# Performance work log

Hardware: AMD Instinct MI355X
Metric: run time of the kernel (lower is better)

## Reference

```python
import jax, jax.numpy as jnp
import numpy as np

EMBED_DIM = 1024
NUM_HEADS = 16
HEAD_DIM = EMBED_DIM // NUM_HEADS


def setup_inputs() -> dict:
    key = jax.random.key(0)
    k1, k2, k3, k4 = jax.random.split(key, 4)
    B, S, D = 2, 2048, EMBED_DIM
    x = jax.random.normal(k1, (B, S, D), dtype=jnp.float32)
    xpos = jax.random.randint(k2, (B, S), 0, 2048, dtype=jnp.int32)
    # torch nn.Linear weights: [out_features, in_features]; qkv_bias=False -> no qkv bias
    qkv_w = jax.random.normal(k3, (3 * D, D), dtype=jnp.float32) * (D ** -0.5)
    proj_w = jax.random.normal(k4, (D, D), dtype=jnp.float32) * (D ** -0.5)
    proj_b = jnp.zeros((D,), dtype=jnp.float32)
    return {"x": x, "xpos": xpos, "qkv_w": qkv_w, "proj_w": proj_w, "proj_b": proj_b}


def reference(x, xpos, qkv_w, proj_w, proj_b):
    # rope is None, dropout rates are 0, so xpos is unused and dropout is identity.
    B, S, D = x.shape
    H, hd = NUM_HEADS, D // NUM_HEADS
    scale = hd ** -0.5

    qkv = x @ qkv_w.T                                   # [B, S, 3D]
    qkv = qkv.reshape(B, S, 3, H, hd)
    qkv = jnp.transpose(qkv, (0, 3, 2, 1, 4))           # [B, H, 3, S, hd]
    q, k, v = qkv[:, :, 0], qkv[:, :, 1], qkv[:, :, 2]  # each [B, H, S, hd]

    scores = jnp.einsum("bhqd,bhkd->bhqk", q, k) * scale  # [B, H, S, S]
    probs = jax.nn.softmax(scores, axis=-1)
    out = jnp.einsum("bhqk,bhkd->bhqd", probs, v)         # [B, H, S, hd]

    out = jnp.transpose(out, (0, 2, 1, 3)).reshape(B, S, D)
    out = out @ proj_w.T + proj_b
    return out
```

## Files before the change

### kernel.cpp

```cpp
#include <hip/hip_runtime.h>


typedef __bf16 bf16_8 __attribute__((ext_vector_type(8)));
typedef __bf16 bf16_4 __attribute__((ext_vector_type(4)));
typedef __bf16 bf16_2 __attribute__((ext_vector_type(2)));
typedef float floatx4 __attribute__((ext_vector_type(4)));
typedef float floatx16 __attribute__((ext_vector_type(16)));
typedef unsigned uintx4 __attribute__((ext_vector_type(4)));

#define MFMA16 __builtin_amdgcn_mfma_f32_16x16x32_bf16
#define MFMA32 __builtin_amdgcn_mfma_f32_32x32x16_bf16
#define CSCALE 0.1803368801111204f
#define EXP2R  __builtin_amdgcn_exp2f

__device__ __forceinline__ void gld16(const __bf16* g, __bf16* l) {
    __builtin_amdgcn_global_load_lds(
        (const __attribute__((address_space(1))) void*)g,
        (__attribute__((address_space(3))) void*)l, 16, 0, 0);
}

__device__ __forceinline__ unsigned pk_bf16(float a, float b) {
    bf16_2 t;
    t[0] = (__bf16)a; t[1] = (__bf16)b;
    return __builtin_bit_cast(unsigned, t);
}

__device__ __forceinline__ void pl32swap(unsigned& a, unsigned& b) {
    __asm__ __volatile__("v_permlane32_swap_b32 %0, %1" : "+v"(a), "+v"(b));
}

__global__ __launch_bounds__(256) void cvt_all(
    const float* __restrict__ x, const float* __restrict__ w1,
    const float* __restrict__ w2,
    __bf16* __restrict__ xb, __bf16* __restrict__ w1b, __bf16* __restrict__ w2b)
{
    const int i = blockIdx.x * 256 + threadIdx.x;
    const float* src; __bf16* dst; int off;
    if (i < (1 << 20))                  { src = x;  dst = xb;  off = i; }
    else if (i < (1 << 20) + 786432)    { src = w1; dst = w1b; off = i - (1 << 20); }
    else                                { src = w2; dst = w2b; off = i - (1 << 20) - 786432; }
    float4 v = ((const float4*)src)[off];
    bf16_4 o;
    o[0] = (__bf16)v.x; o[1] = (__bf16)v.y; o[2] = (__bf16)v.z; o[3] = (__bf16)v.w;
    ((bf16_4*)dst)[off] = o;
}

__global__ __launch_bounds__(512) void qkv_gemm(
    const __bf16* __restrict__ X, const __bf16* __restrict__ W,
    __bf16* __restrict__ q_ws, __bf16* __restrict__ k_ws, __bf16* __restrict__ vt_ws)
{
    __shared__ __align__(16) __bf16 S[2][2][128 * 64];

    const int tid = threadIdx.x, lane = tid & 63;
    const int half = tid >> 8, htid = tid & 255;
    const int wvh = (tid >> 6) & 3;
    const int quad = lane >> 4, l15 = lane & 15;
    const int wm = (wvh >> 1) * 64, wn = (wvh & 1) * 64;
    const int m0 = blockIdx.y * 128, n0 = blockIdx.x * 128;
    const int c = n0 >> 10;

    const __bf16* Abase;
    const __bf16* Bbase;
    if (c == 2) { Abase = X + (size_t)m0 * 1024; Bbase = W + (size_t)n0 * 1024; }
    else        { Abase = W + (size_t)n0 * 1024; Bbase = X + (size_t)m0 * 1024; }
    Abase += half * 512;
    Bbase += half * 512;

    __bf16* As = S[half][0];
    __bf16* Bs = S[half][1];
    floatx4 acc[4][4] = {};

    for (int k0 = 0; k0 < 512; k0 += 64) {
        __syncthreads();
#pragma unroll
        for (int it = 0; it < 4; ++it) {
            int cc = it * 256 + htid;
            int row = cc >> 3, kc = cc & 7;
            gld16(Abase + row * 1024 + k0 + ((kc ^ (row & 7)) * 8), &As[cc * 8]);
        }
#pragma unroll
        for (int it = 0; it < 4; ++it) {
            int cc = it * 256 + htid;
            int row = cc >> 3, kc = cc & 7;
            gld16(Bbase + row * 1024 + k0 + ((kc ^ (row & 7)) * 8), &Bs[cc * 8]);
        }
        __syncthreads();

#pragma unroll
        for (int ks = 0; ks < 2; ++ks) {
            bf16_8 af[4], bf[4];
#pragma unroll
            for (int mt = 0; mt < 4; ++mt) {
                int r = wm + mt * 16 + l15;
                af[mt] = *(const bf16_8*)&As[r * 64 + (((ks * 4 + quad) ^ (r & 7)) * 8)];
            }
#pragma unroll
            for (int nt = 0; nt < 4; ++nt) {
                int r = wn + nt * 16 + l15;
                bf[nt] = *(const bf16_8*)&Bs[r * 64 + (((ks * 4 + quad) ^ (r & 7)) * 8)];
            }
#pragma unroll
            for (int mt = 0; mt < 4; ++mt)
#pragma unroll
                for (int nt = 0; nt < 4; ++nt)
                    acc[mt][nt] = MFMA16(af[mt], bf[nt], acc[mt][nt], 0, 0, 0);
        }
    }

    __syncthreads();
    float* comb = (float*)S;
    if (half == 1) {
#pragma unroll
        for (int mt = 0; mt < 4; ++mt)
#pragma unroll
            for (int nt = 0; nt < 4; ++nt)
                *(floatx4*)&comb[((mt * 4 + nt) * 256 + htid) * 4] = acc[mt][nt];
    }
    __syncthreads();
    if (half != 0) return;

#pragma unroll
    for (int mt = 0; mt < 4; ++mt)
#pragma unroll
        for (int nt = 0; nt < 4; ++nt)
            acc[mt][nt] += *(const floatx4*)&comb[((mt * 4 + nt) * 256 + htid) * 4];

    if (c == 2) {
#pragma unroll
        for (int mt = 0; mt < 4; ++mt) {
            const int mbase = m0 + wm + mt * 16 + quad * 4;
            const int b = mbase >> 11, s = mbase & 2047;
#pragma unroll
            for (int nt = 0; nt < 4; ++nt) {
                const int n = n0 + wn + nt * 16 + l15;
                const int h = (n >> 6) & 15, d = n & 63;
                bf16_4 pk;
#pragma unroll
                for (int r = 0; r < 4; ++r) pk[r] = (__bf16)acc[mt][nt][r];
                *(bf16_4*)&vt_ws[((b * 16 + h) * 64 + d) * 2048 + s] = pk;
            }
        }
    } else {
        __bf16* dst = (c == 0) ? q_ws : k_ws;
        const float scale = (c == 1) ? CSCALE : 1.0f;
#pragma unroll
        for (int mt = 0; mt < 4; ++mt) {
            const int nn = n0 + wm + mt * 16 + quad * 4;
            const int h = (nn >> 6) & 15, d0 = nn & 63;
#pragma unroll
            for (int nt = 0; nt < 4; ++nt) {
                const int token = m0 + wn + nt * 16 + l15;
                const int b = token >> 11, s = token & 2047;
                bf16_4 pk;
#pragma unroll
                for (int r = 0; r < 4; ++r) pk[r] = (__bf16)(acc[mt][nt][r] * scale);
                *(bf16_4*)&dst[((b * 16 + h) * 2048 + s) * 64 + d0] = pk;
            }
        }
    }
}

__global__ __launch_bounds__(256) void attn_kernel(
    const __bf16* __restrict__ q_ws, const __bf16* __restrict__ k_ws,
    const __bf16* __restrict__ vt_ws, __bf16* __restrict__ attn_ws)
{
    __shared__ __align__(16) __bf16 Ks [2][64 * 64];
    __shared__ __align__(16) __bf16 Vts[2][64 * 64];

    const int tid = threadIdx.x, lane = tid & 63, w = tid >> 6;
    const int l31 = lane & 31, hi = lane >> 5;
    const int bh = blockIdx.x, qt = blockIdx.y;
    const int q0 = qt * 128;

    const __bf16* qp  = q_ws  + (size_t)bh * (2048 * 64);
    const __bf16* kp  = k_ws  + (size_t)bh * (2048 * 64);
    const __bf16* vtp = vt_ws + (size_t)bh * (64 * 2048);

    const int srow = tid >> 3, skc = tid & 7;
    const int sw   = (skc ^ (srow & 7)) * 8;
    const __bf16* kb = kp  + (size_t)srow * 64 + sw;
    const __bf16* vb = vtp + (size_t)srow * 2048 + sw;
    const int ldsoff = tid * 8;

    bf16_8 qf[4];
    {
        const int qrow = q0 + w * 32 + l31;
#pragma unroll
        for (int s = 0; s < 4; ++s)
            qf[s] = *(const bf16_8*)&qp[qrow * 64 + s * 16 + hi * 8];
    }

    floatx16 oacc[2] = {};
    float lsum = 0.f;

    gld16(kb,             &Ks [0][ldsoff]);
    gld16(kb + 32 * 64,   &Ks [0][ldsoff + 2048]);
    gld16(vb,             &Vts[0][ldsoff]);
    gld16(vb + 32 * 2048, &Vts[0][ldsoff + 2048]);
    __syncthreads();

#pragma unroll 2
    for (int kt = 0; kt < 32; ++kt) {
        const int cur = kt & 1;
        if (kt < 31) {
            const __bf16* kn = kb + (size_t)(kt + 1) * 4096;
            const __bf16* vn = vb + (size_t)(kt + 1) * 64;
            gld16(kn,             &Ks [cur ^ 1][ldsoff]);
            gld16(kn + 32 * 64,   &Ks [cur ^ 1][ldsoff + 2048]);
            gld16(vn,             &Vts[cur ^ 1][ldsoff]);
            gld16(vn + 32 * 2048, &Vts[cur ^ 1][ldsoff + 2048]);
        }
        const __bf16* Kb = Ks[cur];
        const __bf16* Vb = Vts[cur];

        floatx16 sacc[2] = {};
        __builtin_amdgcn_s_setprio(1);
#pragma unroll
        for (int s = 0; s < 4; ++s) {
            const int kc = s * 2 + hi;
#pragma unroll
            for (int t = 0; t < 2; ++t) {
                const int row = t * 32 + l31;
                bf16_8 kf = *(const bf16_8*)&Kb[row * 64 + ((kc ^ (row & 7)) * 8)];
                sacc[t] = MFMA32(kf, qf[s], sacc[t], 0, 0, 0);
            }
        }
        __builtin_amdgcn_s_setprio(0);

        unsigned D[2][4][2];
#pragma unroll
        for (int t = 0; t < 2; ++t)
#pragma unroll
            for (int j = 0; j < 4; ++j)
#pragma unroll
                for (int e = 0; e < 2; ++e) {
                    float pa = EXP2R(sacc[t][j * 4 + e * 2]);
                    float pb = EXP2R(sacc[t][j * 4 + e * 2 + 1]);
                    lsum += pa + pb;
                    D[t][j][e] = pk_bf16(pa, pb);
                }

        __builtin_amdgcn_s_setprio(1);
#pragma unroll
        for (int s = 0; s < 4; ++s) {
            const int t = s >> 1, b2 = (s & 1) * 2;
            unsigned x0 = D[t][b2][0], y0 = D[t][b2 + 1][0];
            unsigned x1 = D[t][b2][1], y1 = D[t][b2 + 1][1];
            pl32swap(x0, y0);
            pl32swap(x1, y1);
            uintx4 u; u[0] = x0; u[1] = x1; u[2] = y0; u[3] = y1;
            const bf16_8 pf = __builtin_bit_cast(bf16_8, u);
            const int kc = s * 2 + hi;
#pragma unroll
            for (int dt = 0; dt < 2; ++dt) {
                const int row = dt * 32 + l31;
                bf16_8 vf = *(const bf16_8*)&Vb[row * 64 + ((kc ^ (row & 7)) * 8)];
                oacc[dt] = MFMA32(vf, pf, oacc[dt], 0, 0, 0);
            }
        }
        __builtin_amdgcn_s_setprio(0);

        if (kt < 31) {
            __asm__ __volatile__("s_waitcnt vmcnt(0)" ::: "memory");
            __syncthreads();
        }
    }

    const int b = bh >> 4, h = bh & 15;
    const float lpart = __shfl_xor(lsum, 32, 64);
    const float inv_l = 1.0f / (lsum + lpart);
    const int token = b * 2048 + q0 + w * 32 + l31;
#pragma unroll
    for (int dt = 0; dt < 2; ++dt)
#pragma unroll
        for (int g = 0; g < 4; ++g) {
            bf16_4 ok;
#pragma unroll
            for (int r = 0; r < 4; ++r)
                ok[r] = (__bf16)(oacc[dt][g * 4 + r] * inv_l);
            *(bf16_4*)&attn_ws[(size_t)token * 1024 + h * 64 + dt * 32 + g * 8 + hi * 4] = ok;
        }
}

__device__ __forceinline__ void proj_stage(
    const __bf16* __restrict__ A, const __bf16* __restrict__ Bp,
    int k0, __bf16* As, __bf16* Bs, int tid)
{
#pragma unroll
    for (int it = 0; it < 4; ++it) {
        int cc = it * 256 + tid;
        int row = cc >> 3, kc = cc & 7;
        gld16(A + row * 1024 + k0 + ((kc ^ (row & 7)) * 8), &As[cc * 8]);
    }
#pragma unroll
    for (int it = 0; it < 2; ++it) {
        int cc = it * 256 + tid;
        int row = cc >> 3, kc = cc & 7;
        gld16(Bp + row * 1024 + k0 + ((kc ^ (row & 7)) * 8), &Bs[cc * 8]);
    }
}

__global__ __launch_bounds__(256) void proj_gemm(
    const __bf16* __restrict__ Ain, const __bf16* __restrict__ W,
    const float* __restrict__ bias, float* __restrict__ out)
{
    __shared__ __align__(16) __bf16 As[2][128 * 64];
    __shared__ __align__(16) __bf16 Bs[2][64 * 64];
    floatx4 acc[4][2] = {};
    const int m0 = blockIdx.y * 128, n0 = blockIdx.x * 64;

    const int tid = threadIdx.x, lane = tid & 63, wv = tid >> 6;
    const int quad = lane >> 4, l15 = lane & 15;
    const int wm = (wv >> 1) * 64, wn = (wv & 1) * 32;

    const __bf16* A  = Ain + (size_t)m0 * 1024;
    const __bf16* Bp = W   + (size_t)n0 * 1024;

    proj_stage(A, Bp, 0, As[0], Bs[0], tid);
    __syncthreads();

#pragma unroll 2
    for (int kk = 0; kk < 16; ++kk) {
        const int cur = kk & 1;
        if (kk < 15)
            proj_stage(A, Bp, (kk + 1) * 64, As[cur ^ 1], Bs[cur ^ 1], tid);

        const __bf16* Ab = As[cur];
        const __bf16* Bb = Bs[cur];
#pragma unroll
        for (int ks = 0; ks < 2; ++ks) {
            bf16_8 af[4], bf[2];
#pragma unroll
            for (int mt = 0; mt < 4; ++mt) {
                int r = wm + mt * 16 + l15;
                af[mt] = *(const bf16_8*)&Ab[r * 64 + (((ks * 4 + quad) ^ (r & 7)) * 8)];
            }
#pragma unroll
            for (int nt = 0; nt < 2; ++nt) {
                int r = wn + nt * 16 + l15;
                bf[nt] = *(const bf16_8*)&Bb[r * 64 + (((ks * 4 + quad) ^ (r & 7)) * 8)];
            }
#pragma unroll
            for (int mt = 0; mt < 4; ++mt)
#pragma unroll
                for (int nt = 0; nt < 2; ++nt)
                    acc[mt][nt] = MFMA16(af[mt], bf[nt], acc[mt][nt], 0, 0, 0);
        }

        if (kk < 15) {
            __asm__ __volatile__("s_waitcnt vmcnt(0)" ::: "memory");
            __syncthreads();
        }
    }

    float bv[2];
#pragma unroll
    for (int nt = 0; nt < 2; ++nt) bv[nt] = bias[n0 + wn + nt * 16 + l15];

#pragma unroll
    for (int mt = 0; mt < 4; ++mt) {
        const int m = m0 + wm + mt * 16 + quad * 4;
#pragma unroll
        for (int nt = 0; nt < 2; ++nt) {
            const int n = n0 + wn + nt * 16 + l15;
#pragma unroll
            for (int r = 0; r < 4; ++r)
                out[(size_t)(m + r) * 1024 + n] = acc[mt][nt][r] + bv[nt];
        }
    }
}

extern "C" void kernel_launch(void* const* d_in, const int* in_sizes, int n_in,
                              void* d_out, int out_size, void* d_ws, size_t ws_size,
                              hipStream_t stream)
{
    const float* x      = (const float*)d_in[0];
    const float* qkv_w  = (const float*)d_in[2];
    const float* proj_w = (const float*)d_in[3];
    const float* proj_b = (const float*)d_in[4];
    float* out = (float*)d_out;

    const size_t SZ   = 4096 * 1024;
    const size_t WQKV = 3072 * 1024;
    const size_t WPRJ = 1024 * 1024;

    __bf16* xb      = (__bf16*)d_ws;
    __bf16* qkvwb   = xb + SZ;
    __bf16* projwb  = qkvwb + WQKV;
    __bf16* q_ws    = projwb + WPRJ;
    __bf16* k_ws    = q_ws + SZ;
    __bf16* vt_ws   = k_ws + SZ;
    __bf16* attn_ws = vt_ws + SZ;

    cvt_all<<<dim3(8192), 256, 0, stream>>>(x, qkv_w, proj_w, xb, qkvwb, projwb);
    qkv_gemm  <<<dim3(24, 32), 512, 0, stream>>>(xb, qkvwb, q_ws, k_ws, vt_ws);
    attn_kernel<<<dim3(32, 16), 256, 0, stream>>>(q_ws, k_ws, vt_ws, attn_ws);
    proj_gemm <<<dim3(16, 32), 256, 0, stream>>>(attn_ws, projwb, proj_b, out);
}
```

Baseline: 188.6 us.

## Pre-swizzle K/V into MFMA fragment layout and load directly to registers

The QKV GEMM now writes K and V^T in a layout that matches the per-lane MFMA operand fragments. The attention kernel can then read K and V straight from global memory into registers, with K software-pipelined one tile ahead, instead of staging them through LDS behind barriers. The QKV GEMM also drops its two-half split-K design with an LDS reduction in favour of a 256-thread double-buffered K loop. The attention grid is reordered so consecutive blocks share the same head. In exchange, every wave loads its own copy of K and V from global/L2 with no LDS sharing, and register pressure rises.

New measurement: 182.3 us. 3.4% less time.

```diff
diff --git a/kernel.cpp b/kernel.cpp
--- a/kernel.cpp
+++ b/kernel.cpp
@@ -45,17 +45,15 @@
     ((bf16_4*)dst)[off] = o;
 }
 
-__global__ __launch_bounds__(512) void qkv_gemm(
+__global__ __launch_bounds__(256) void qkv_gemm(
     const __bf16* __restrict__ X, const __bf16* __restrict__ W,
     __bf16* __restrict__ q_ws, __bf16* __restrict__ k_ws, __bf16* __restrict__ vt_ws)
 {
     __shared__ __align__(16) __bf16 S[2][2][128 * 64];
 
-    const int tid = threadIdx.x, lane = tid & 63;
-    const int half = tid >> 8, htid = tid & 255;
-    const int wvh = (tid >> 6) & 3;
+    const int tid = threadIdx.x, lane = tid & 63, wv = tid >> 6;
     const int quad = lane >> 4, l15 = lane & 15;
-    const int wm = (wvh >> 1) * 64, wn = (wvh & 1) * 64;
+    const int wm = (wv >> 1) * 64, wn = (wv & 1) * 64;
     const int m0 = blockIdx.y * 128, n0 = blockIdx.x * 128;
     const int c = n0 >> 10;
 
@@ -63,29 +61,32 @@
     const __bf16* Bbase;
     if (c == 2) { Abase = X + (size_t)m0 * 1024; Bbase = W + (size_t)n0 * 1024; }
     else        { Abase = W + (size_t)n0 * 1024; Bbase = X + (size_t)m0 * 1024; }
-    Abase += half * 512;
-    Bbase += half * 512;
-
-    __bf16* As = S[half][0];
-    __bf16* Bs = S[half][1];
+
+    const int srow = tid >> 3, skc = tid & 7;
+    const int ssw  = (skc ^ (srow & 7)) * 8;
+
+#define QKV_STAGE(buf, k0)                                                     \
+    {                                                                          \
+        _Pragma("unroll")                                                      \
+        for (int itg = 0; itg < 4; ++itg) {                                    \
+            const int cc = itg * 256 + tid;                                    \
+            const int row = srow + itg * 32;                                   \
+            gld16(Abase + row * 1024 + (k0) + ssw, &S[buf][0][cc * 8]);        \
+            gld16(Bbase + row * 1024 + (k0) + ssw, &S[buf][1][cc * 8]);        \
+        }                                                                      \
+    }
+
     floatx4 acc[4][4] = {};
-
-    for (int k0 = 0; k0 < 512; k0 += 64) {
-        __syncthreads();
-#pragma unroll
-        for (int it = 0; it < 4; ++it) {
-            int cc = it * 256 + htid;
-            int row = cc >> 3, kc = cc & 7;
-            gld16(Abase + row * 1024 + k0 + ((kc ^ (row & 7)) * 8), &As[cc * 8]);
-        }
-#pragma unroll
-        for (int it = 0; it < 4; ++it) {
-            int cc = it * 256 + htid;
-            int row = cc >> 3, kc = cc & 7;
-            gld16(Bbase + row * 1024 + k0 + ((kc ^ (row & 7)) * 8), &Bs[cc * 8]);
-        }
-        __syncthreads();
-
+    QKV_STAGE(0, 0)
+    __syncthreads();
+
+#pragma unroll 1
+    for (int kk = 0; kk < 16; ++kk) {
+        const int cur = kk & 1;
+        if (kk < 15) QKV_STAGE(cur ^ 1, (kk + 1) * 64)
+
+        const __bf16* As = S[cur][0];
+        const __bf16* Bs = S[cur][1];
 #pragma unroll
         for (int ks = 0; ks < 2; ++ks) {
             bf16_8 af[4], bf[4];
@@ -105,43 +106,34 @@
                 for (int nt = 0; nt < 4; ++nt)
                     acc[mt][nt] = MFMA16(af[mt], bf[nt], acc[mt][nt], 0, 0, 0);
         }
-    }
-
-    __syncthreads();
-    float* comb = (float*)S;
-    if (half == 1) {
-#pragma unroll
-        for (int mt = 0; mt < 4; ++mt)
-#pragma unroll
-            for (int nt = 0; nt < 4; ++nt)
-                *(floatx4*)&comb[((mt * 4 + nt) * 256 + htid) * 4] = acc[mt][nt];
-    }
-    __syncthreads();
-    if (half != 0) return;
-
-#pragma unroll
-    for (int mt = 0; mt < 4; ++mt)
-#pragma unroll
-        for (int nt = 0; nt < 4; ++nt)
-            acc[mt][nt] += *(const floatx4*)&comb[((mt * 4 + nt) * 256 + htid) * 4];
+
+        if (kk < 15) {
+            __asm__ __volatile__("s_waitcnt vmcnt(0)" ::: "memory");
+            __syncthreads();
+        }
+    }
 
     if (c == 2) {
 #pragma unroll
         for (int mt = 0; mt < 4; ++mt) {
             const int mbase = m0 + wm + mt * 16 + quad * 4;
-            const int b = mbase >> 11, s = mbase & 2047;
+            const int b = mbase >> 11, key0 = mbase & 2047;
 #pragma unroll
             for (int nt = 0; nt < 4; ++nt) {
                 const int n = n0 + wn + nt * 16 + l15;
                 const int h = (n >> 6) & 15, d = n & 63;
+                const int dt = d >> 5, l31v = d & 31;
                 bf16_4 pk;
 #pragma unroll
                 for (int r = 0; r < 4; ++r) pk[r] = (__bf16)acc[mt][nt][r];
-                *(bf16_4*)&vt_ws[((b * 16 + h) * 64 + d) * 2048 + s] = pk;
+                const size_t off =
+                    (((size_t)(b * 16 + h) * 32 + (key0 >> 6)) * 2 + dt) * 2048
+                    + ((key0 >> 4) & 3) * 512
+                    + (((key0 >> 3) & 1) * 32 + l31v) * 8 + (key0 & 7);
+                *(bf16_4*)&vt_ws[off] = pk;
             }
         }
     } else {
-        __bf16* dst = (c == 0) ? q_ws : k_ws;
         const float scale = (c == 1) ? CSCALE : 1.0f;
 #pragma unroll
         for (int mt = 0; mt < 4; ++mt) {
@@ -150,37 +142,37 @@
 #pragma unroll
             for (int nt = 0; nt < 4; ++nt) {
                 const int token = m0 + wn + nt * 16 + l15;
-                const int b = token >> 11, s = token & 2047;
+                const int b = token >> 11, key = token & 2047;
                 bf16_4 pk;
 #pragma unroll
                 for (int r = 0; r < 4; ++r) pk[r] = (__bf16)(acc[mt][nt][r] * scale);
-                *(bf16_4*)&dst[((b * 16 + h) * 2048 + s) * 64 + d0] = pk;
-            }
-        }
-    }
+                if (c == 0) {
+                    *(bf16_4*)&q_ws[((size_t)(b * 16 + h) * 2048 + key) * 64 + d0] = pk;
+                } else {
+                    const size_t off =
+                        (((size_t)(b * 16 + h) * 32 + (key >> 6)) * 2 + ((key >> 5) & 1)) * 2048
+                        + (d0 >> 4) * 512
+                        + (((d0 >> 3) & 1) * 32 + (key & 31)) * 8 + (d0 & 7);
+                    *(bf16_4*)&k_ws[off] = pk;
+                }
+            }
+        }
+    }
+#undef QKV_STAGE
 }
 
 __global__ __launch_bounds__(256) void attn_kernel(
     const __bf16* __restrict__ q_ws, const __bf16* __restrict__ k_ws,
     const __bf16* __restrict__ vt_ws, __bf16* __restrict__ attn_ws)
 {
-    __shared__ __align__(16) __bf16 Ks [2][64 * 64];
-    __shared__ __align__(16) __bf16 Vts[2][64 * 64];
-
     const int tid = threadIdx.x, lane = tid & 63, w = tid >> 6;
     const int l31 = lane & 31, hi = lane >> 5;
-    const int bh = blockIdx.x, qt = blockIdx.y;
+    const int qt = blockIdx.x, bh = blockIdx.y;
     const int q0 = qt * 128;
 
-    const __bf16* qp  = q_ws  + (size_t)bh * (2048 * 64);
-    const __bf16* kp  = k_ws  + (size_t)bh * (2048 * 64);
-    const __bf16* vtp = vt_ws + (size_t)bh * (64 * 2048);
-
-    const int srow = tid >> 3, skc = tid & 7;
-    const int sw   = (skc ^ (srow & 7)) * 8;
-    const __bf16* kb = kp  + (size_t)srow * 64 + sw;
-    const __bf16* vb = vtp + (size_t)srow * 2048 + sw;
-    const int ldsoff = tid * 8;
+    const __bf16* qp  = q_ws + (size_t)bh * (2048 * 64);
+    const __bf16* kfn = k_ws  + (size_t)bh * 131072 + lane * 8;
+    const __bf16* vfp = vt_ws + (size_t)bh * 131072 + lane * 8;
 
     bf16_8 qf[4];
     {
@@ -193,78 +185,64 @@
     floatx16 oacc[2] = {};
     float lsum = 0.f;
 
-    gld16(kb,             &Ks [0][ldsoff]);
-    gld16(kb + 32 * 64,   &Ks [0][ldsoff + 2048]);
-    gld16(vb,             &Vts[0][ldsoff]);
-    gld16(vb + 32 * 2048, &Vts[0][ldsoff + 2048]);
-    __syncthreads();
-
-#pragma unroll 2
-    for (int kt = 0; kt < 32; ++kt) {
-        const int cur = kt & 1;
-        if (kt < 31) {
-            const __bf16* kn = kb + (size_t)(kt + 1) * 4096;
-            const __bf16* vn = vb + (size_t)(kt + 1) * 64;
-            gld16(kn,             &Ks [cur ^ 1][ldsoff]);
-            gld16(kn + 32 * 64,   &Ks [cur ^ 1][ldsoff + 2048]);
-            gld16(vn,             &Vts[cur ^ 1][ldsoff]);
-            gld16(vn + 32 * 2048, &Vts[cur ^ 1][ldsoff + 2048]);
-        }
-        const __bf16* Kb = Ks[cur];
-        const __bf16* Vb = Vts[cur];
-
-        floatx16 sacc[2] = {};
-        __builtin_amdgcn_s_setprio(1);
-#pragma unroll
-        for (int s = 0; s < 4; ++s) {
-            const int kc = s * 2 + hi;
-#pragma unroll
-            for (int t = 0; t < 2; ++t) {
-                const int row = t * 32 + l31;
-                bf16_8 kf = *(const bf16_8*)&Kb[row * 64 + ((kc ^ (row & 7)) * 8)];
-                sacc[t] = MFMA32(kf, qf[s], sacc[t], 0, 0, 0);
-            }
-        }
-        __builtin_amdgcn_s_setprio(0);
-
-        unsigned D[2][4][2];
-#pragma unroll
-        for (int t = 0; t < 2; ++t)
-#pragma unroll
-            for (int j = 0; j < 4; ++j)
-#pragma unroll
-                for (int e = 0; e < 2; ++e) {
-                    float pa = EXP2R(sacc[t][j * 4 + e * 2]);
-                    float pb = EXP2R(sacc[t][j * 4 + e * 2 + 1]);
-                    lsum += pa + pb;
-                    D[t][j][e] = pk_bf16(pa, pb);
-                }
-
-        __builtin_amdgcn_s_setprio(1);
-#pragma unroll
-        for (int s = 0; s < 4; ++s) {
-            const int t = s >> 1, b2 = (s & 1) * 2;
-            unsigned x0 = D[t][b2][0], y0 = D[t][b2 + 1][0];
-            unsigned x1 = D[t][b2][1], y1 = D[t][b2 + 1][1];
-            pl32swap(x0, y0);
-            pl32swap(x1, y1);
-            uintx4 u; u[0] = x0; u[1] = x1; u[2] = y0; u[3] = y1;
-            const bf16_8 pf = __builtin_bit_cast(bf16_8, u);
-            const int kc = s * 2 + hi;
-#pragma unroll
-            for (int dt = 0; dt < 2; ++dt) {
-                const int row = dt * 32 + l31;
-                bf16_8 vf = *(const bf16_8*)&Vb[row * 64 + ((kc ^ (row & 7)) * 8)];
-                oacc[dt] = MFMA32(vf, pf, oacc[dt], 0, 0, 0);
-            }
-        }
-        __builtin_amdgcn_s_setprio(0);
-
-        if (kt < 31) {
-            __asm__ __volatile__("s_waitcnt vmcnt(0)" ::: "memory");
-            __syncthreads();
-        }
-    }
+    bf16_8 ka[8], kb[8], va[8];
+#pragma unroll
+    for (int u = 0; u < 8; ++u)
+        ka[u] = *(const bf16_8*)&kfn[(u >> 2) * 2048 + (u & 3) * 512];
+    kfn += 4096;
+
+#define ATTN_TILE(KC, KN)                                                      \
+    {                                                                          \
+        _Pragma("unroll")                                                      \
+        for (int u = 0; u < 8; ++u)       \
+            va[u] = *(const bf16_8*)&vfp[(u >> 2) * 2048 + (u & 3) * 512];     \
+        floatx16 sacc[2] = {};                                                 \
+        __builtin_amdgcn_s_setprio(1);                                         \
+        _Pragma("unroll")                                                      \
+        for (int s = 0; s < 4; ++s) {                                          \
+            sacc[0] = MFMA32(KC[s],     qf[s], sacc[0], 0, 0, 0);              \
+            sacc[1] = MFMA32(KC[4 + s], qf[s], sacc[1], 0, 0, 0);              \
+        }                                                                      \
+        __builtin_amdgcn_s_setprio(0);                                         \
+        _Pragma("unroll")                                                      \
+        for (int u = 0; u < 8; ++u)                       \
+            KN[u] = *(const bf16_8*)&kfn[(u >> 2) * 2048 + (u & 3) * 512];     \
+        unsigned D[2][4][2];                                                   \
+        _Pragma("unroll")                                                      \
+        for (int t = 0; t < 2; ++t)                                            \
+            _Pragma("unroll")                                                  \
+            for (int j = 0; j < 4; ++j)                                        \
+                _Pragma("unroll")                                              \
+                for (int e = 0; e < 2; ++e) {                                  \
+                    float pa = EXP2R(sacc[t][j * 4 + e * 2]);                  \
+                    float pb = EXP2R(sacc[t][j * 4 + e * 2 + 1]);              \
+                    lsum += pa + pb;                                           \
+                    D[t][j][e] = pk_bf16(pa, pb);                              \
+                }                                                              \
+        __builtin_amdgcn_s_setprio(1);                                         \
+        _Pragma("unroll")                                                      \
+        for (int s = 0; s < 4; ++s) {                                          \
+            const int t = s >> 1, b2 = (s & 1) * 2;                            \
+            unsigned x0 = D[t][b2][0], y0 = D[t][b2 + 1][0];                   \
+            unsigned x1 = D[t][b2][1], y1 = D[t][b2 + 1][1];                   \
+            pl32swap(x0, y0);                                                  \
+            pl32swap(x1, y1);                                                  \
+            uintx4 uu; uu[0] = x0; uu[1] = x1; uu[2] = y0; uu[3] = y1;         \
+            const bf16_8 pf = __builtin_bit_cast(bf16_8, uu);                  \
+            oacc[0] = MFMA32(va[s],     pf, oacc[0], 0, 0, 0);                 \
+            oacc[1] = MFMA32(va[4 + s], pf, oacc[1], 0, 0, 0);                 \
+        }                                                                      \
+        __builtin_amdgcn_s_setprio(0);                                         \
+        vfp += 4096;                                                           \
+        kfn += 4096;                                                           \
+    }
+
+#pragma unroll 1
+    for (int it = 0; it < 16; ++it) {
+        ATTN_TILE(ka, kb)
+        ATTN_TILE(kb, ka)
+    }
+#undef ATTN_TILE
 
     const int b = bh >> 4, h = bh & 15;
     const float lpart = __shfl_xor(lsum, 32, 64);
@@ -393,7 +371,7 @@
     __bf16* attn_ws = vt_ws + SZ;
 
     cvt_all<<<dim3(8192), 256, 0, stream>>>(x, qkv_w, proj_w, xb, qkvwb, projwb);
-    qkv_gemm  <<<dim3(24, 32), 512, 0, stream>>>(xb, qkvwb, q_ws, k_ws, vt_ws);
-    attn_kernel<<<dim3(32, 16), 256, 0, stream>>>(q_ws, k_ws, vt_ws, attn_ws);
+    qkv_gemm  <<<dim3(24, 32), 256, 0, stream>>>(xb, qkvwb, q_ws, k_ws, vt_ws);
+    attn_kernel<<<dim3(16, 32), 256, 0, stream>>>(q_ws, k_ws, vt_ws, attn_ws);
     proj_gemm <<<dim3(16, 32), 256, 0, stream>>>(attn_ws, projwb, proj_b, out);
 }
```
